# Optimization experiments

Hardware: AMD Instinct MI355X
Metric: run time of the kernel (lower is better)

Reference implementation:

```python
import jax, jax.numpy as jnp
import numpy as np

EPS = 1e-5
HEADS, DK, DV = 8, 32, 32


def conv3x3(x, w, b):
    # regular (non-depthwise, despite the name) 3x3 conv, stride 1, padding 1
    y = jax.lax.conv_general_dilated(
        x, w, window_strides=(1, 1), padding='SAME',
        dimension_numbers=('NCHW', 'OIHW', 'NCHW'))
    return y + b[None, :, None, None]


def setup_inputs() -> dict:
    key = jax.random.key(0)
    ks = jax.random.split(key, 16)
    C = 256
    d = {}
    d['x'] = jax.random.normal(ks[0], (8, C, 32, 32), jnp.float32)
    s_lin = 1.0 / np.sqrt(C)
    s_conv = 1.0 / np.sqrt(C * 9)
    d['Wq'] = jax.random.normal(ks[1], (C, HEADS * DK), jnp.float32) * s_lin
    d['bq'] = jnp.zeros((HEADS * DK,), jnp.float32)
    d['conv_k_w'] = jax.random.normal(ks[2], (C, C, 3, 3), jnp.float32) * s_conv
    d['conv_k_b'] = jnp.zeros((C,), jnp.float32)
    d['Wk'] = jax.random.normal(ks[3], (C, HEADS * DK), jnp.float32) * s_lin
    d['bk'] = jnp.zeros((HEADS * DK,), jnp.float32)
    d['conv_v_w'] = jax.random.normal(ks[4], (C, C, 3, 3), jnp.float32) * s_conv
    d['conv_v_b'] = jnp.zeros((C,), jnp.float32)
    d['Wv'] = jax.random.normal(ks[5], (C, HEADS * DV), jnp.float32) * s_lin
    d['bv'] = jnp.zeros((HEADS * DV,), jnp.float32)
    d['Wo'] = jax.random.normal(ks[6], (HEADS * DV, C), jnp.float32) * s_lin
    d['bo'] = jnp.zeros((C,), jnp.float32)
    d['B'] = jax.random.normal(ks[7], (1, HEADS, 1024, 1024), jnp.float32) * 0.02
    return d


def reference(x, Wq, bq, conv_k_w, conv_k_b, Wk, bk, conv_v_w, conv_v_b, Wv, bv, Wo, bo, B):
    b, c, h, w = x.shape
    hw = h * w
    xr = x.reshape(b, c, hw).transpose(0, 2, 1)  # [b, hw, c]
    # F.layer_norm with normalized_shape == full shape: whole-tensor stats, no affine
    m = jnp.mean(xr)
    v = jnp.mean((xr - m) ** 2)
    xn = (xr - m) * jax.lax.rsqrt(v + EPS)

    q = (xn @ Wq + bq).reshape(b, hw, HEADS, DK).transpose(0, 2, 1, 3)  # [b,H,hw,dk]

    k = conv3x3(x, conv_k_w, conv_k_b)  # stride 1 -> same spatial size (per source)
    k = k.reshape(b, c, hw).transpose(0, 2, 1)
    k = (k @ Wk + bk).reshape(b, hw, HEADS, DK).transpose(0, 2, 1, 3)

    vv = conv3x3(x, conv_v_w, conv_v_b)
    vv = vv.reshape(b, c, hw).transpose(0, 2, 1)
    vv = (vv @ Wv + bv).reshape(b, hw, HEADS, DV).transpose(0, 2, 1, 3)

    scale = DK ** (-0.5)
    attn = jnp.einsum('bhid,bhjd->bhij', q, k) * scale + B  # [b,H,hw,hw]
    attn = jax.nn.softmax(attn, axis=-1)
    out = jnp.einsum('bhij,bhjd->bhid', attn, vv)  # [b,H,hw,dv]
    out = out.transpose(0, 2, 1, 3).reshape(b, hw, HEADS * DV)
    out = out @ Wo + bo  # [b, hw, c]
    # faithful to torch .view(b, c, h, w): raw reshape, NO transpose
    out = out.reshape(b, c, h, w)
    return out + x
```

## Files before the change

kernel.cpp:

```cpp
#include <hip/hip_runtime.h>
#include <hip/hip_bf16.h>
#include <math.h>

#define B_     8
#define C_     256
#define HW_    1024
#define NTOT   (B_*C_*HW_)
#define HEADS_ 8
#define DK_    32
#define SCALE_ 0.17677669529663687f
#define L2E_   1.4426950408889634f

#define F_STATS 0
#define F_PART  16
#define F_YK2   8192
#define F_YV2   (F_YK2 + NTOT)
#define F_XB    (F_YV2 + NTOT)
#define F_WT    (F_XB + NTOT/2)
#define F_QB    (F_WT + 589824)
#define F_KB    (F_QB + NTOT/2)
#define F_VT    (F_KB + NTOT/2)
#define F_WT4   (F_VT + NTOT/2)
#define F_BETA0 (F_WT4 + 131072)

typedef float f32x4 __attribute__((ext_vector_type(4)));
typedef short short8 __attribute__((ext_vector_type(8)));

__device__ __forceinline__ short bf16s(float f) {
    __hip_bfloat16 h = __float2bfloat16(f);
    return *(short*)&h;
}
__device__ __forceinline__ unsigned pack_bf16(float a, float b) {
    unsigned ua = (unsigned short)bf16s(a);
    unsigned ub = (unsigned short)bf16s(b);
    return ua | (ub << 16);
}
__device__ __forceinline__ void gload_lds16(const short* g, short* l) {
    __builtin_amdgcn_global_load_lds(
        (const __attribute__((address_space(1))) unsigned*)g,
        (__attribute__((address_space(3))) unsigned*)l, 16, 0, 0);
}

__global__ void k_prep_all(const float* __restrict__ x,
                           const float* __restrict__ wk, const float* __restrict__ wv,
                           const float* __restrict__ Wq, const float* __restrict__ Wk,
                           const float* __restrict__ Wv, const float* __restrict__ Wo,
                           short* __restrict__ xb, float* __restrict__ part,
                           short* __restrict__ wt, short* __restrict__ wt4) {
    __shared__ short t[32 * 258];
    __shared__ float ls[4], ls2[4];
    int bid = blockIdx.x;
    int tid = threadIdx.x;
    if (bid < 256) {
        int b = bid >> 5, p0 = (bid & 31) << 5;
        float s = 0.f, s2 = 0.f;
        for (int i = tid; i < 256 * 32; i += 256) {
            int ci = i >> 5, p = i & 31;
            float v = x[(b * C_ + ci) * HW_ + p0 + p];
            s += v; s2 += v * v;
            t[p * 258 + ci] = bf16s(v);
        }
        for (int o = 32; o; o >>= 1) { s += __shfl_down(s, o); s2 += __shfl_down(s2, o); }
        int wid = tid >> 6, lane = tid & 63;
        if (lane == 0) { ls[wid] = s; ls2[wid] = s2; }
        __syncthreads();
        if (tid == 0) {
            float a = 0.f, bb = 0.f;
            for (int i = 0; i < 4; i++) { a += ls[i]; bb += ls2[i]; }
            part[bid * 2] = a; part[bid * 2 + 1] = bb;
        }
        for (int i = tid; i < 32 * 256; i += 256) {
            int p = i >> 8, ci = i & 255;
            xb[(b * HW_ + p0 + p) * C_ + ci] = t[p * 258 + ci];
        }
    } else if (bid < 1408) {
        int idx = (bid - 256) * 256 + tid;
        int ci0 = (idx << 2) & 255;
        int rest = idx >> 6;
        int n = rest & 511, tap = rest >> 9;
        const float* src = (n < 256) ? (wk + (n * C_) * 9) : (wv + ((n - 256) * C_) * 9);
        short4 o;
        short* op = (short*)&o;
        for (int u = 0; u < 4; u++)
            op[u] = bf16s(src[(ci0 + u) * 9 + tap]);
        *(short4*)&wt[((tap * 512 + n) * C_) + ci0] = o;
    } else {
        int b2 = bid - 1408;
        int mi = b2 >> 4, tl = b2 & 15;
        int c0 = (tl >> 2) * 64, e0 = (tl & 3) * 64;
        const float* W = mi == 0 ? Wq : mi == 1 ? Wk : mi == 2 ? Wv : Wo;
        for (int i = tid; i < 4096; i += 256) {
            int cl = i >> 6, el = i & 63;
            t[cl * 66 + el] = bf16s(W[(c0 + cl) * 256 + e0 + el]);
        }
        __syncthreads();
        for (int i = tid; i < 4096; i += 256) {
            int el = i >> 6, cl = i & 63;
            wt4[mi * 65536 + (e0 + el) * 256 + c0 + cl] = t[cl * 66 + el];
        }
    }
}

__global__ void k_stats_beta(const float* __restrict__ part,
                             const float* __restrict__ Wq, const float* __restrict__ bq,
                             float* __restrict__ stats, float* __restrict__ beta0) {
    __shared__ float ls[256], ls2[256], ps[1024], st2[2];
    int tid = threadIdx.x;
    if (tid < 256) { ls[tid] = part[2 * tid]; ls2[tid] = part[2 * tid + 1]; }
    __syncthreads();
    for (int off = 128; off; off >>= 1) {
        if (tid < off) { ls[tid] += ls[tid + off]; ls2[tid] += ls2[tid + off]; }
        __syncthreads();
    }
    if (tid == 0) {
        float m = ls[0] / (float)NTOT;
        float var = ls2[0] / (float)NTOT - m * m;
        float r = rsqrtf(var + 1e-5f);
        stats[0] = m; stats[1] = r;
        st2[0] = m; st2[1] = r;
    }
    int e = tid & 255, pp = tid >> 8;
    float s = 0.f;
    for (int c = pp * 64; c < pp * 64 + 64; c++) s += Wq[c * 256 + e];
    ps[tid] = s;
    __syncthreads();
    if (tid < 256) {
        float cs = ps[tid] + ps[tid + 256] + ps[tid + 512] + ps[tid + 768];
        beta0[tid] = (bq[tid] - st2[0] * st2[1] * cs) * SCALE_;
    }
}

__device__ __forceinline__ int a_off(int slot, int chunk) {
    int c = chunk ^ (slot & 3);
    int s = slot ^ ((slot >> 2) & 1);
    return s * 64 + c * 16;
}

__global__ __launch_bounds__(512, 4)
void k_conv_mfma(const short* __restrict__ xb, const short* __restrict__ wt,
                 const float* __restrict__ bk, const float* __restrict__ bv,
                 short* __restrict__ yk2b, short* __restrict__ yv2b) {
    __shared__ short a_sh[204 * 32];
    __shared__ short b_sh[9 * 2048];
    int bid = blockIdx.x;
    int nt = bid & 7, pt = (bid >> 3) & 7, b = bid >> 6;
    int R0 = pt * 4;
    int tid = threadIdx.x;
    int w = tid >> 6, l = tid & 63;
    int wm = w >> 1, wn = w & 1;
    int col16 = l & 15, kq = l >> 4;

    int offs[2], loffs[2];
    #pragma unroll
    for (int it = 0; it < 2; it++) {
        int i = tid + it * 512;
        if (i < 816) {
            int slot = i >> 2, chunk = i & 3;
            int ty = slot / 34, tx = slot - ty * 34;
            int Y = R0 - 1 + ty, X = tx - 1;
            offs[it] = ((unsigned)Y < 32u && (unsigned)X < 32u)
                       ? ((b * HW_ + Y * 32 + X) * C_ + chunk * 8) : -1;
            loffs[it] = a_off(slot, chunk);
        } else { offs[it] = -1; loffs[it] = -1; }
    }

    int bgoff[5];
    int nbj = 0;
    #pragma unroll 1
    for (int j = w; j < 36; j += 8) {
        int S = j * 64 + l;
        int tap = S >> 8, s = S & 255;
        int colb = s >> 2, kqs = s & 3;
        int kq2 = kqs ^ ((colb >> 1) & 3);
        bgoff[nbj++] = (tap * 512 + nt * 64 + colb) * C_ + kq2 * 8;
    }

    f32x4 acc[2][2];
    #pragma unroll
    for (int m = 0; m < 2; m++)
        #pragma unroll
        for (int n = 0; n < 2; n++) acc[m][n] = (f32x4)0.f;

    int sr[2];
    #pragma unroll
    for (int nf = 0; nf < 2; nf++) {
        int colb = wn * 32 + nf * 16 + col16;
        sr[nf] = (colb << 2) | (kq ^ ((colb >> 1) & 3));
    }

    {
        short8 sv[2];
        #pragma unroll
        for (int it = 0; it < 2; it++)
            sv[it] = (offs[it] >= 0) ? *(const short8*)(xb + offs[it]) : (short8)0;
        int jj = 0;
        #pragma unroll 1
        for (int j = w; j < 36; j += 8, jj++)
            gload_lds16(wt + bgoff[jj], b_sh + j * 512);
        #pragma unroll
        for (int it = 0; it < 2; it++)
            if (loffs[it] >= 0) *(short8*)((char*)a_sh + loffs[it]) = sv[it];
    }
    __syncthreads();

    #pragma unroll 1
    for (int step = 0; step < 8; step++) {
        const char* ab = (const char*)a_sh;
        const char* bbp = (const char*)b_sh;
        #pragma unroll
        for (int tap = 0; tap < 9; tap++) {
            const int dyi = tap / 3, dxi = tap % 3;
            short8 af[2], bf[2];
            #pragma unroll
            for (int mf = 0; mf < 2; mf++) {
                int slot = (wm + dyi) * 34 + mf * 16 + col16 + dxi;
                af[mf] = *(const short8*)(ab + a_off(slot, kq));
            }
            #pragma unroll
            for (int nf = 0; nf < 2; nf++)
                bf[nf] = *(const short8*)(bbp + tap * 4096 + sr[nf] * 16);
            #pragma unroll
            for (int mf = 0; mf < 2; mf++)
                #pragma unroll
                for (int nf = 0; nf < 2; nf++)
                    acc[mf][nf] = __builtin_amdgcn_mfma_f32_16x16x32_bf16(af[mf], bf[nf], acc[mf][nf], 0, 0, 0);
        }
        if (step < 7) {
            int ci0n = step * 32 + 32;
            __syncthreads();
            short8 sv[2];
            #pragma unroll
            for (int it = 0; it < 2; it++)
                sv[it] = (offs[it] >= 0) ? *(const short8*)(xb + offs[it] + ci0n) : (short8)0;
            int jj = 0;
            #pragma unroll 1
            for (int j = w; j < 36; j += 8, jj++)
                gload_lds16(wt + bgoff[jj] + ci0n, b_sh + j * 512);
            #pragma unroll
            for (int it = 0; it < 2; it++)
                if (loffs[it] >= 0) *(short8*)((char*)a_sh + loffs[it]) = sv[it];
            __syncthreads();
        }
    }

    const bool isv = (nt >= 4);
    short* dst = isv ? yv2b : yk2b;
    const float* bias = isv ? bv : bk;
    int cbase = (nt & 3) * 64 + wn * 32 + col16;
    #pragma unroll
    for (int nf = 0; nf < 2; nf++) {
        int co = cbase + nf * 16;
        float bi = bias[co];
        #pragma unroll
        for (int mf = 0; mf < 2; mf++) {
            #pragma unroll
            for (int r = 0; r < 4; r++) {
                int pixel = pt * 128 + wm * 32 + mf * 16 + kq * 4 + r;
                dst[(b * HW_ + pixel) * C_ + co] = bf16s(acc[mf][nf][r] + bi);
            }
        }
    }
}

__global__ void k_proj_mfma(const short* __restrict__ xb,
                            const short* __restrict__ yk2b, const short* __restrict__ yv2b,
                            const short* __restrict__ wt4,
                            const float* __restrict__ bkp, const float* __restrict__ bvp,
                            const float* __restrict__ stats, const float* __restrict__ beta0,
                            short* __restrict__ qb, short* __restrict__ kb,
                            short* __restrict__ vt) {
    __shared__ char smem[17408];
    int pj = blockIdx.x, pt = blockIdx.y, b = blockIdx.z;
    int p0 = pt * 32;
    int tid = threadIdx.x, w = tid >> 6, l = tid & 63;
    int c16 = l & 15, kq = l >> 4;

    const short* src = pj == 0 ? xb : (pj == 1 ? yk2b : yv2b);
    #pragma unroll
    for (int it = 0; it < 4; it++) {
        int i = it * 256 + tid;
        int slab = i >> 7, rem = i & 127, slot = rem >> 2, chunk = rem & 3;
        short8 v = *(const short8*)(src + ((b * HW_ + p0 + slot) * C_ + slab * 32 + chunk * 8));
        *(short8*)(smem + slab * 2048 + a_off(slot, chunk)) = v;
    }
    __syncthreads();

    const short* wt_p = wt4 + pj * 65536;
    f32x4 acc[2][4];
    #pragma unroll
    for (int m = 0; m < 2; m++)
        #pragma unroll
        for (int n = 0; n < 4; n++) acc[m][n] = (f32x4)0.f;

    for (int s = 0; s < 8; s++) {
        short8 af[2], bf[4];
        #pragma unroll
        for (int mf = 0; mf < 2; mf++)
            af[mf] = *(const short8*)(smem + s * 2048 + a_off(mf * 16 + c16, kq));
        #pragma unroll
        for (int nf = 0; nf < 4; nf++)
            bf[nf] = *(const short8*)(wt_p + (w * 64 + nf * 16 + c16) * 256 + s * 32 + kq * 8);
        #pragma unroll
        for (int mf = 0; mf < 2; mf++)
            #pragma unroll
            for (int nf = 0; nf < 4; nf++)
                acc[mf][nf] = __builtin_amdgcn_mfma_f32_16x16x32_bf16(af[mf], bf[nf], acc[mf][nf], 0, 0, 0);
    }

    float alpha = (pj == 0) ? stats[1] * SCALE_ : 1.f;
    float beta[4];
    #pragma unroll
    for (int nf = 0; nf < 4; nf++) {
        int e = w * 64 + nf * 16 + c16;
        beta[nf] = (pj == 0) ? beta0[e] : (pj == 1 ? bkp[e] : bvp[e]);
    }
    __syncthreads();

    short* rp = (short*)smem + w * 2176;
    if (pj < 2) {
        #pragma unroll
        for (int mf = 0; mf < 2; mf++)
            #pragma unroll
            for (int nf = 0; nf < 4; nf++)
                #pragma unroll
                for (int rg = 0; rg < 4; rg++) {
                    int px = mf * 16 + kq * 4 + rg, el = nf * 16 + c16;
                    rp[px * 66 + el] = bf16s(alpha * acc[mf][nf][rg] + beta[nf]);
                }
        __syncthreads();
        short* dst = (pj == 0) ? qb : kb;
        #pragma unroll
        for (int j = 0; j < 4; j++) {
            int px = j * 8 + (l >> 3), el = (l & 7) * 8;
            short8 v = *(const short8*)(rp + px * 66 + el);
            int e = w * 64 + el, h = e >> 5, d = e & 31;
            *(short8*)(dst + ((b * 8 + h) * HW_ + p0 + px) * DK_ + d) = v;
        }
    } else {
        #pragma unroll
        for (int mf = 0; mf < 2; mf++)
            #pragma unroll
            for (int nf = 0; nf < 4; nf++)
                #pragma unroll
                for (int rg = 0; rg < 4; rg++) {
                    int px = mf * 16 + kq * 4 + rg, el = nf * 16 + c16;
                    rp[el * 34 + px] = bf16s(acc[mf][nf][rg] + beta[nf]);
                }
        __syncthreads();
        #pragma unroll
        for (int j = 0; j < 4; j++) {
            int el = j * 16 + (l >> 2), px = (l & 3) * 8;
            short8 v = *(const short8*)(rp + el * 34 + px);
            int e = w * 64 + el, h = e >> 5, d = e & 31;
            *(short8*)(vt + ((b * 8 + h) * DK_ + d) * HW_ + p0 + px) = v;
        }
    }
}

__global__ __launch_bounds__(256, 4)
void k_attn(const short* __restrict__ qb, const short* __restrict__ kb,
            const short* __restrict__ vt, const float* __restrict__ Bb,
            short* __restrict__ ao) {
    __shared__ __align__(16) short Ks[128 * 32];
    __shared__ __align__(16) short Vs[32 * 128];
    int bid = blockIdx.x;
    int h = bid & 7, b = (bid >> 3) & 7, qt = bid >> 6;
    int bh = b * HEADS_ + h;
    int tid = threadIdx.x, w = tid >> 6, l = tid & 63;
    int g = l >> 4, c16 = l & 15;

    int qrow = qt * 64 + w * 16 + c16;
    short8 qf = *(const short8*)(qb + (bh * HW_ + qrow) * DK_ + g * 8);
    const float* Brow = Bb + (h * HW_ + qrow) * HW_;

    float4 breg[8];
    #pragma unroll
    for (int mt = 0; mt < 8; mt++)
        breg[mt] = *(const float4*)(Brow + mt * 16 + g * 4);

    float m_run = -1e30f, l_run = 0.f;
    f32x4 ot[2];
    ot[0] = (f32x4)0.f; ot[1] = (f32x4)0.f;

    int vrow = tid >> 4, vch = tid & 15;
    int vrow2 = (tid + 256) >> 4, vch2 = (tid + 256) & 15;
    const short* kbase = kb + bh * HW_ * DK_;

    for (int kv0 = 0; kv0 < HW_; kv0 += 128) {
        __syncthreads();
        gload_lds16(kbase + kv0 * DK_ + (w * 2) * 512 + l * 8, Ks + (w * 2) * 512);
        gload_lds16(kbase + kv0 * DK_ + (w * 2 + 1) * 512 + l * 8, Ks + (w * 2 + 1) * 512);
        {
            short8 v0 = *(const short8*)(vt + (bh * DK_ + vrow) * HW_ + kv0 + vch * 8);
            short8 v1 = *(const short8*)(vt + (bh * DK_ + vrow2) * HW_ + kv0 + vch2 * 8);
            *(short8*)((char*)Vs + vrow * 256 + ((vch * 16) ^ ((vrow & 7) << 4))) = v0;
            *(short8*)((char*)Vs + vrow2 * 256 + ((vch2 * 16) ^ ((vrow2 & 7) << 4))) = v1;
        }
        __syncthreads();

        f32x4 st[8];
        __builtin_amdgcn_s_setprio(1);
        #pragma unroll
        for (int mt = 0; mt < 8; mt++) {
            f32x4 acc;
            acc[0] = breg[mt].x; acc[1] = breg[mt].y; acc[2] = breg[mt].z; acc[3] = breg[mt].w;
            short8 kf = *(const short8*)(Ks + (mt * 16 + c16) * DK_ + g * 8);
            st[mt] = __builtin_amdgcn_mfma_f32_16x16x32_bf16(kf, qf, acc, 0, 0, 0);
        }
        __builtin_amdgcn_s_setprio(0);
        if (kv0 + 128 < HW_) {
            #pragma unroll
            for (int mt = 0; mt < 8; mt++)
                breg[mt] = *(const float4*)(Brow + kv0 + 128 + mt * 16 + g * 4);
        }

        float pmax = st[0][0];
        #pragma unroll
        for (int mt = 0; mt < 8; mt++)
            #pragma unroll
            for (int rg = 0; rg < 4; rg++) pmax = fmaxf(pmax, st[mt][rg]);
        pmax = fmaxf(pmax, __shfl_xor(pmax, 16));
        pmax = fmaxf(pmax, __shfl_xor(pmax, 32));
        if (!__all(pmax <= m_run + 8.f)) {
            float mnew = fmaxf(m_run, pmax);
            float f = exp2f((m_run - mnew) * L2E_);
            m_run = mnew;
            l_run *= f;
            int fv = __float_as_int(f);
            #pragma unroll
            for (int rg = 0; rg < 4; rg++) {
                float fr = __int_as_float(__builtin_amdgcn_ds_bpermute((g * 4 + rg) << 2, fv));
                ot[0][rg] *= fr;
                ot[1][rg] *= fr;
            }
        }
        float negml = -m_run * L2E_;
        float s = 0.f;
        #pragma unroll
        for (int mt = 0; mt < 8; mt++)
            #pragma unroll
            for (int rg = 0; rg < 4; rg++) {
                float e_ = exp2f(fmaf(st[mt][rg], L2E_, negml));
                st[mt][rg] = e_;
                s += e_;
            }
        s += __shfl_xor(s, 16);
        s += __shfl_xor(s, 32);
        l_run += s;

        short8 pa[4];
        #pragma unroll
        for (int kt = 0; kt < 4; kt++) {
            unsigned u0 = pack_bf16(st[2 * kt][0], st[2 * kt][1]);
            unsigned u1 = pack_bf16(st[2 * kt][2], st[2 * kt][3]);
            unsigned u2 = pack_bf16(st[2 * kt + 1][0], st[2 * kt + 1][1]);
            unsigned u3 = pack_bf16(st[2 * kt + 1][2], st[2 * kt + 1][3]);
            unsigned* pu = (unsigned*)&pa[kt];
            pu[0] = u0; pu[1] = u1; pu[2] = u2; pu[3] = u3;
        }

        __builtin_amdgcn_s_setprio(1);
        #pragma unroll
        for (int kt = 0; kt < 4; kt++) {
            #pragma unroll
            for (int nt = 0; nt < 2; nt++) {
                int dv = c16 + 16 * nt;
                int X0 = kt * 64 + 8 * g;
                int X1 = X0 + 32;
                int a0 = dv * 256 + ((((X0 >> 4) ^ (dv & 7)) << 4) | (X0 & 15));
                int a1 = dv * 256 + ((((X1 >> 4) ^ (dv & 7)) << 4) | (X1 & 15));
                unsigned long long lo = *(const unsigned long long*)((char*)Vs + a0);
                unsigned long long hi = *(const unsigned long long*)((char*)Vs + a1);
                short8 vf;
                *(unsigned long long*)&vf = lo;
                *((unsigned long long*)&vf + 1) = hi;
                ot[nt] = __builtin_amdgcn_mfma_f32_16x16x32_bf16(pa[kt], vf, ot[nt], 0, 0, 0);
            }
        }
        __builtin_amdgcn_s_setprio(0);
    }

    float linv = 1.f / l_run;
    int lrv = __float_as_int(linv);
    #pragma unroll
    for (int rg = 0; rg < 4; rg++) {
        float li = __int_as_float(__builtin_amdgcn_ds_bpermute((g * 4 + rg) << 2, lrv));
        int qg = qt * 64 + w * 16 + g * 4 + rg;
        #pragma unroll
        for (int nt = 0; nt < 2; nt++)
            ao[(b * HW_ + qg) * C_ + h * DK_ + nt * 16 + c16] = bf16s(ot[nt][rg] * li);
    }
}

__global__ void k_out_mfma(const short* __restrict__ aob, const short* __restrict__ wot,
                           const float* __restrict__ bo, const float* __restrict__ x,
                           float* __restrict__ out) {
    __shared__ char smem[16384];
    int pt = blockIdx.x, b = blockIdx.y;
    int p0 = pt * 32;
    int tid = threadIdx.x, w = tid >> 6, l = tid & 63;
    int c16 = l & 15, kq = l >> 4;

    #pragma unroll
    for (int it = 0; it < 4; it++) {
        int i = it * 256 + tid;
        int slab = i >> 7, rem = i & 127, slot = rem >> 2, chunk = rem & 3;
        short8 v = *(const short8*)(aob + ((b * HW_ + p0 + slot) * C_ + slab * 32 + chunk * 8));
        *(short8*)(smem + slab * 2048 + a_off(slot, chunk)) = v;
    }
    __syncthreads();

    f32x4 acc[2][4];
    #pragma unroll
    for (int m = 0; m < 2; m++)
        #pragma unroll
        for (int n = 0; n < 4; n++) acc[m][n] = (f32x4)0.f;

    for (int s = 0; s < 8; s++) {
        short8 af[2], bf[4];
        #pragma unroll
        for (int mf = 0; mf < 2; mf++)
            af[mf] = *(const short8*)(smem + s * 2048 + a_off(mf * 16 + c16, kq));
        #pragma unroll
        for (int nf = 0; nf < 4; nf++)
            bf[nf] = *(const short8*)(wot + (w * 64 + nf * 16 + c16) * 256 + s * 32 + kq * 8);
        #pragma unroll
        for (int mf = 0; mf < 2; mf++)
            #pragma unroll
            for (int nf = 0; nf < 4; nf++)
                acc[mf][nf] = __builtin_amdgcn_mfma_f32_16x16x32_bf16(af[mf], bf[nf], acc[mf][nf], 0, 0, 0);
    }

    #pragma unroll
    for (int nf = 0; nf < 4; nf++) {
        int e = w * 64 + nf * 16 + c16;
        float bov = bo[e];
        #pragma unroll
        for (int mf = 0; mf < 2; mf++) {
            #pragma unroll
            for (int rg = 0; rg < 4; rg++) {
                int px = mf * 16 + kq * 4 + rg;
                int idx = b * (C_ * HW_) + (p0 + px) * 256 + e;
                out[idx] = acc[mf][nf][rg] + bov + x[idx];
            }
        }
    }
}

extern "C" void kernel_launch(void* const* d_in, const int* in_sizes, int n_in,
                              void* d_out, int out_size, void* d_ws, size_t ws_size,
                              hipStream_t stream) {
    const float* x   = (const float*)d_in[0];
    const float* Wq  = (const float*)d_in[1];
    const float* bq  = (const float*)d_in[2];
    const float* ckw = (const float*)d_in[3];
    const float* ckb = (const float*)d_in[4];
    const float* Wk  = (const float*)d_in[5];
    const float* bk  = (const float*)d_in[6];
    const float* cvw = (const float*)d_in[7];
    const float* cvb = (const float*)d_in[8];
    const float* Wv  = (const float*)d_in[9];
    const float* bv  = (const float*)d_in[10];
    const float* Wo  = (const float*)d_in[11];
    const float* bo  = (const float*)d_in[12];
    const float* Bb  = (const float*)d_in[13];
    float* ws  = (float*)d_ws;
    float* out = (float*)d_out;

    short* xb      = (short*)(ws + F_XB);
    short* wt      = (short*)(ws + F_WT);
    short* wt4     = (short*)(ws + F_WT4);
    float* beta0   = ws + F_BETA0;
    short* qb      = (short*)(ws + F_QB);
    short* kb      = (short*)(ws + F_KB);
    short* vt      = (short*)(ws + F_VT);
    short* yk2b    = (short*)(ws + F_YK2);
    short* yv2b    = (short*)(ws + F_YV2);
    short* aob     = (short*)(ws + F_YK2);
    short* wot     = wt4 + 3 * 65536;

    k_prep_all  <<<1472, 256, 0, stream>>>(x, ckw, cvw, Wq, Wk, Wv, Wo,
                                           xb, ws + F_PART, wt, wt4);
    k_stats_beta<<<1,   1024, 0, stream>>>(ws + F_PART, Wq, bq, ws + F_STATS, beta0);
    k_conv_mfma <<<512,  512, 0, stream>>>(xb, wt, ckb, cvb, yk2b, yv2b);
    k_proj_mfma <<<dim3(3, 32, 8), 256, 0, stream>>>(xb, yk2b, yv2b,
                                                     wt4, bk, bv, ws + F_STATS, beta0,
                                                     qb, kb, vt);
    k_attn      <<<1024, 256, 0, stream>>>(qb, kb, vt, Bb, aob);
    k_out_mfma  <<<dim3(32, 8), 256, 0, stream>>>(aob, wot, bo, x, out);
}
```

Measured before the change: 126.8 us.

## Halve conv output-channel tile, double grid, and switch softmax to __expf

The conv kernel's per-block output-channel tile shrinks from 64 to 32 channels and the grid doubles to 1024 blocks. Each wave now computes one 16-pixel M fragment times two N fragments, and the launch-bounds occupancy hint rises from 4 to 8. This raises occupancy and parallelism but halves reuse of the A tile, which each block now reloads for fewer output channels. Separately, the attention softmax replaces exp2f with a pre-multiplied log2(e) by __expf on the difference from the running max, which may cost an extra multiply per element.

New measurement: 128.0 us. No clear change (+0.9%).

```diff
diff --git a/kernel.cpp b/kernel.cpp
--- a/kernel.cpp
+++ b/kernel.cpp
@@ -9,7 +9,6 @@
 #define HEADS_ 8
 #define DK_    32
 #define SCALE_ 0.17677669529663687f
-#define L2E_   1.4426950408889634f
 
 #define F_STATS 0
 #define F_PART  16
@@ -136,18 +135,17 @@
     return s * 64 + c * 16;
 }
 
-__global__ __launch_bounds__(512, 4)
+__global__ __launch_bounds__(512, 8)
 void k_conv_mfma(const short* __restrict__ xb, const short* __restrict__ wt,
                  const float* __restrict__ bk, const float* __restrict__ bv,
                  short* __restrict__ yk2b, short* __restrict__ yv2b) {
     __shared__ short a_sh[204 * 32];
-    __shared__ short b_sh[9 * 2048];
+    __shared__ short b_sh[9 * 1024];
     int bid = blockIdx.x;
-    int nt = bid & 7, pt = (bid >> 3) & 7, b = bid >> 6;
+    int nt = bid & 15, pt = (bid >> 4) & 7, b = bid >> 7;
     int R0 = pt * 4;
     int tid = threadIdx.x;
     int w = tid >> 6, l = tid & 63;
-    int wm = w >> 1, wn = w & 1;
     int col16 = l & 15, kq = l >> 4;
 
     int offs[2], loffs[2];
@@ -164,27 +162,24 @@
         } else { offs[it] = -1; loffs[it] = -1; }
     }
 
-    int bgoff[5];
+    int bgoff[3];
     int nbj = 0;
     #pragma unroll 1
-    for (int j = w; j < 36; j += 8) {
+    for (int j = w; j < 18; j += 8) {
         int S = j * 64 + l;
-        int tap = S >> 8, s = S & 255;
+        int tap = S >> 7, s = S & 127;
         int colb = s >> 2, kqs = s & 3;
         int kq2 = kqs ^ ((colb >> 1) & 3);
-        bgoff[nbj++] = (tap * 512 + nt * 64 + colb) * C_ + kq2 * 8;
-    }
-
-    f32x4 acc[2][2];
-    #pragma unroll
-    for (int m = 0; m < 2; m++)
-        #pragma unroll
-        for (int n = 0; n < 2; n++) acc[m][n] = (f32x4)0.f;
+        bgoff[nbj++] = (tap * 512 + nt * 32 + colb) * C_ + kq2 * 8;
+    }
+
+    f32x4 acc[2];
+    acc[0] = (f32x4)0.f; acc[1] = (f32x4)0.f;
 
     int sr[2];
     #pragma unroll
     for (int nf = 0; nf < 2; nf++) {
-        int colb = wn * 32 + nf * 16 + col16;
+        int colb = nf * 16 + col16;
         sr[nf] = (colb << 2) | (kq ^ ((colb >> 1) & 3));
     }
 
@@ -195,7 +190,7 @@
             sv[it] = (offs[it] >= 0) ? *(const short8*)(xb + offs[it]) : (short8)0;
         int jj = 0;
         #pragma unroll 1
-        for (int j = w; j < 36; j += 8, jj++)
+        for (int j = w; j < 18; j += 8, jj++)
             gload_lds16(wt + bgoff[jj], b_sh + j * 512);
         #pragma unroll
         for (int it = 0; it < 2; it++)
@@ -203,6 +198,7 @@
     }
     __syncthreads();
 
+    int prow = w >> 1, pcol = (w & 1) * 16 + col16;
     #pragma unroll 1
     for (int step = 0; step < 8; step++) {
         const char* ab = (const char*)a_sh;
@@ -210,20 +206,15 @@
         #pragma unroll
         for (int tap = 0; tap < 9; tap++) {
             const int dyi = tap / 3, dxi = tap % 3;
-            short8 af[2], bf[2];
-            #pragma unroll
-            for (int mf = 0; mf < 2; mf++) {
-                int slot = (wm + dyi) * 34 + mf * 16 + col16 + dxi;
-                af[mf] = *(const short8*)(ab + a_off(slot, kq));
-            }
+            int slot = (prow + dyi) * 34 + pcol + dxi;
+            short8 af = *(const short8*)(ab + a_off(slot, kq));
+            short8 bf[2];
             #pragma unroll
             for (int nf = 0; nf < 2; nf++)
-                bf[nf] = *(const short8*)(bbp + tap * 4096 + sr[nf] * 16);
-            #pragma unroll
-            for (int mf = 0; mf < 2; mf++)
-                #pragma unroll
-                for (int nf = 0; nf < 2; nf++)
-                    acc[mf][nf] = __builtin_amdgcn_mfma_f32_16x16x32_bf16(af[mf], bf[nf], acc[mf][nf], 0, 0, 0);
+                bf[nf] = *(const short8*)(bbp + tap * 2048 + sr[nf] * 16);
+            #pragma unroll
+            for (int nf = 0; nf < 2; nf++)
+                acc[nf] = __builtin_amdgcn_mfma_f32_16x16x32_bf16(af, bf[nf], acc[nf], 0, 0, 0);
         }
         if (step < 7) {
             int ci0n = step * 32 + 32;
@@ -234,7 +225,7 @@
                 sv[it] = (offs[it] >= 0) ? *(const short8*)(xb + offs[it] + ci0n) : (short8)0;
             int jj = 0;
             #pragma unroll 1
-            for (int j = w; j < 36; j += 8, jj++)
+            for (int j = w; j < 18; j += 8, jj++)
                 gload_lds16(wt + bgoff[jj] + ci0n, b_sh + j * 512);
             #pragma unroll
             for (int it = 0; it < 2; it++)
@@ -243,21 +234,18 @@
         }
     }
 
-    const bool isv = (nt >= 4);
+    const bool isv = (nt >= 8);
     short* dst = isv ? yv2b : yk2b;
     const float* bias = isv ? bv : bk;
-    int cbase = (nt & 3) * 64 + wn * 32 + col16;
+    int cbase = (nt & 7) * 32 + col16;
     #pragma unroll
     for (int nf = 0; nf < 2; nf++) {
         int co = cbase + nf * 16;
         float bi = bias[co];
         #pragma unroll
-        for (int mf = 0; mf < 2; mf++) {
-            #pragma unroll
-            for (int r = 0; r < 4; r++) {
-                int pixel = pt * 128 + wm * 32 + mf * 16 + kq * 4 + r;
-                dst[(b * HW_ + pixel) * C_ + co] = bf16s(acc[mf][nf][r] + bi);
-            }
+        for (int r = 0; r < 4; r++) {
+            int pixel = pt * 128 + w * 16 + kq * 4 + r;
+            dst[(b * HW_ + pixel) * C_ + co] = bf16s(acc[nf][r] + bi);
         }
     }
 }
@@ -423,7 +411,7 @@
         pmax = fmaxf(pmax, __shfl_xor(pmax, 32));
         if (!__all(pmax <= m_run + 8.f)) {
             float mnew = fmaxf(m_run, pmax);
-            float f = exp2f((m_run - mnew) * L2E_);
+            float f = __expf(m_run - mnew);
             m_run = mnew;
             l_run *= f;
             int fv = __float_as_int(f);
@@ -434,13 +422,12 @@
                 ot[1][rg] *= fr;
             }
         }
-        float negml = -m_run * L2E_;
         float s = 0.f;
         #pragma unroll
         for (int mt = 0; mt < 8; mt++)
             #pragma unroll
             for (int rg = 0; rg < 4; rg++) {
-                float e_ = exp2f(fmaf(st[mt][rg], L2E_, negml));
+                float e_ = __expf(st[mt][rg] - m_run);
                 st[mt][rg] = e_;
                 s += e_;
             }
@@ -582,7 +569,7 @@
     k_prep_all  <<<1472, 256, 0, stream>>>(x, ckw, cvw, Wq, Wk, Wv, Wo,
                                            xb, ws + F_PART, wt, wt4);
     k_stats_beta<<<1,   1024, 0, stream>>>(ws + F_PART, Wq, bq, ws + F_STATS, beta0);
-    k_conv_mfma <<<512,  512, 0, stream>>>(xb, wt, ckb, cvb, yk2b, yv2b);
+    k_conv_mfma <<<1024, 512, 0, stream>>>(xb, wt, ckb, cvb, yk2b, yv2b);
     k_proj_mfma <<<dim3(3, 32, 8), 256, 0, stream>>>(xb, yk2b, yv2b,
                                                      wt4, bk, bv, ws + F_STATS, beta0,
                                                      qb, kb, vt);
```
